# Performance work log

Measured on AMD Instinct MI355X. Metric: run time of the kernel, lower is better.

## Reference

```python
import jax, jax.numpy as jnp
import numpy as np

B, S, E, H, VS, VT = 128, 256, 512, 512, 32000, 32000


def _lstm_layer(x, mask, Wih, Whh, bih, bhh):
    # x: (S,B,E_in), mask: (S,B) bool. PyTorch gate order i,f,g,o.
    h0 = jnp.zeros((x.shape[1], Whh.shape[1]), x.dtype)
    c0 = h0
    def step(carry, inp):
        h, c = carry
        xt, mt = inp
        g = xt @ Wih.T + h @ Whh.T + bih + bhh
        i, f, gg, o = jnp.split(g, 4, axis=-1)
        i = jax.nn.sigmoid(i); f = jax.nn.sigmoid(f)
        gg = jnp.tanh(gg); o = jax.nn.sigmoid(o)
        c_new = f * c + i * gg
        h_new = o * jnp.tanh(c_new)
        m = mt[:, None]
        h2 = jnp.where(m, h_new, h)
        c2 = jnp.where(m, c_new, c)
        return (h2, c2), jnp.where(m, h_new, 0.0)  # pad_packed zero-pads
    (hT, cT), ys = jax.lax.scan(step, (h0, c0), (x, mask))
    return ys, cT


def setup_inputs() -> dict:
    key = jax.random.key(0)
    ks = jax.random.split(key, 32)
    def w(k, shape, fan_in):
        bound = 1.0 / np.sqrt(fan_in)
        return jax.random.uniform(k, shape, jnp.float32, -bound, bound)
    src_tokens = jax.random.randint(ks[0], (B, S), 0, VS)
    src_lens = jnp.sort(jax.random.randint(ks[1], (B,), S // 2, S + 1))[::-1]
    src_lens = src_lens.at[0].set(S)  # pack_padded expects descending, max = S
    trg_tokens = jax.random.randint(ks[2], (B,), 0, VT)
    inp = {
        'src_tokens': src_tokens, 'src_lens': src_lens, 'trg_tokens': trg_tokens,
        'src_emb': jax.random.normal(ks[3], (VS, E), jnp.float32),
        'trg_emb': jax.random.normal(ks[4], (VT, E), jnp.float32),
        'enc_Wih0': w(ks[5], (4 * H, E), H), 'enc_Whh0': w(ks[6], (4 * H, H), H),
        'enc_bih0': w(ks[7], (4 * H,), H), 'enc_bhh0': w(ks[8], (4 * H,), H),
        'enc_Wih1': w(ks[9], (4 * H, H), H), 'enc_Whh1': w(ks[10], (4 * H, H), H),
        'enc_bih1': w(ks[11], (4 * H,), H), 'enc_bhh1': w(ks[12], (4 * H,), H),
        'dec_Wih': w(ks[13], (4 * H, E + H), H), 'dec_Whh': w(ks[14], (4 * H, H), H),
        'dec_bih': w(ks[15], (4 * H,), H), 'dec_bhh': w(ks[16], (4 * H,), H),
        'W_init': w(ks[17], (H, 2 * H), 2 * H), 'b_init': w(ks[18], (H,), 2 * H),
        'W_hid': w(ks[19], (H, 2 * H), 2 * H), 'b_hid': w(ks[20], (H,), 2 * H),
        'W_out': w(ks[21], (VT, H), H), 'b_out': w(ks[22], (VT,), H),
    }
    return inp


def reference(src_tokens, src_lens, trg_tokens, src_emb, trg_emb,
              enc_Wih0, enc_Whh0, enc_bih0, enc_bhh0,
              enc_Wih1, enc_Whh1, enc_bih1, enc_bhh1,
              dec_Wih, dec_Whh, dec_bih, dec_bhh,
              W_init, b_init, W_hid, b_hid, W_out, b_out):
    # ---- encode ----
    x = src_emb[src_tokens]                       # (B,S,E)
    x = jnp.transpose(x, (1, 0, 2))               # (S,B,E)
    mask = jnp.arange(S)[:, None] < src_lens[None, :]  # (S,B)
    y0, c0f = _lstm_layer(x, mask, enc_Wih0, enc_Whh0, enc_bih0, enc_bhh0)
    y1, c1f = _lstm_layer(y0, mask, enc_Wih1, enc_Whh1, enc_bih1, enc_bhh1)
    src_states = jnp.transpose(y1, (1, 0, 2))     # (B,S,H)
    # final cell states (num_layers,B,H) -> (B, num_layers*H)
    final_cells = jnp.concatenate([c0f, c1f], axis=-1)  # (B,2H)
    c_dec = final_cells @ W_init.T + b_init       # (B,H)
    h_dec = jnp.tanh(c_dec)
    # ---- one decoder step ----
    emb_t = trg_emb[trg_tokens]                   # (B,E)
    vec = jnp.concatenate([emb_t, jnp.zeros((B, H), emb_t.dtype)], axis=-1)
    g = vec @ dec_Wih.T + h_dec @ dec_Whh.T + dec_bih + dec_bhh
    i, f, gg, o = jnp.split(g, 4, axis=-1)
    c = jax.nn.sigmoid(f) * c_dec + jax.nn.sigmoid(i) * jnp.tanh(gg)
    h = jax.nn.sigmoid(o) * jnp.tanh(c)           # (B,H)
    # ---- masked dot attention ----
    scores = jnp.einsum('bsh,bh->bs', src_states, h)
    smask = jnp.arange(S)[None, :] < src_lens[:, None]
    scores = jnp.where(smask, scores, -jnp.inf)
    attw = jax.nn.softmax(scores, axis=-1)
    context = jnp.einsum('bs,bsh->bh', attw, src_states)
    attn_vec = jnp.concatenate([h, context], axis=-1) @ W_hid.T + b_hid
    logits = attn_vec @ W_out.T + b_out
    prd_token = jnp.argmax(logits, axis=-1)       # softmax is monotone
    return context, h, prd_token
```

## Files before the change

kernel.cpp:

```cpp
#include <hip/hip_runtime.h>
#include <stdint.h>


typedef _Float16 f16;
typedef f16 f16x8 __attribute__((ext_vector_type(8)));
typedef float f32x4 __attribute__((ext_vector_type(4)));

#define LOSCALE 2048.0f
#define LOINV   (1.0f/2048.0f)

#define B_  128
#define S_  256
#define H_  512

__device__ __forceinline__ uint16_t hbits(f16 h){ union{ f16 f; uint16_t u; } c; c.f=h; return c.u; }

__device__ __forceinline__ uint32_t split_ph2(float x){
  f16 h = (f16)x;
  float r = (x - (float)h) * LOSCALE;
  return (uint32_t)hbits(h) | ((uint32_t)hbits((f16)r) << 16);
}
__device__ __forceinline__ float ph2val(uint32_t p){
  union{ uint16_t u; f16 f; } a, b; a.u = (uint16_t)p; b.u = (uint16_t)(p>>16);
  return (float)a.f + (float)b.f * LOINV;
}

__device__ __forceinline__ void pack_hi_lo(const uint4& a, const uint4& b, uint4& hi, uint4& lo){
  hi = make_uint4((a.x & 0xffffu) | (a.y << 16),
                  (a.z & 0xffffu) | (a.w << 16),
                  (b.x & 0xffffu) | (b.y << 16),
                  (b.z & 0xffffu) | (b.w << 16));
  lo = make_uint4((a.x >> 16) | (a.y & 0xffff0000u),
                  (a.z >> 16) | (a.w & 0xffff0000u),
                  (b.x >> 16) | (b.y & 0xffff0000u),
                  (b.z >> 16) | (b.w & 0xffff0000u));
}

__device__ __forceinline__ void split_pack8(const float* x, uint4& hi, uint4& lo){
  uint16_t h[8], l[8];
#pragma unroll
  for (int e = 0; e < 8; ++e) {
    f16 hh = (f16)x[e];
    float r = (x[e] - (float)hh) * LOSCALE;
    h[e] = hbits(hh); l[e] = hbits((f16)r);
  }
  hi = make_uint4((uint32_t)h[0]|((uint32_t)h[1]<<16), (uint32_t)h[2]|((uint32_t)h[3]<<16),
                  (uint32_t)h[4]|((uint32_t)h[5]<<16), (uint32_t)h[6]|((uint32_t)h[7]<<16));
  lo = make_uint4((uint32_t)l[0]|((uint32_t)l[1]<<16), (uint32_t)l[2]|((uint32_t)l[3]<<16),
                  (uint32_t)l[4]|((uint32_t)l[5]<<16), (uint32_t)l[6]|((uint32_t)l[7]<<16));
}

__device__ __forceinline__ f32x4 mfma16(uint4 a, uint4 b, f32x4 c){
  return __builtin_amdgcn_mfma_f32_16x16x32_f16(
      __builtin_bit_cast(f16x8, a), __builtin_bit_cast(f16x8, b), c, 0, 0, 0);
}

__device__ __forceinline__ float sigm(float x){ return 1.0f/(1.0f + expf(-x)); }
__device__ __forceinline__ float fsigm(float x){ return 1.0f/(1.0f + __expf(-x)); }
__device__ __forceinline__ float ftanh(float x){
  float ax = fabsf(x);
  float e = __expf(-2.0f*ax);
  float r = (1.0f - e)/(1.0f + e);
  return copysignf(r, x);
}

__device__ __forceinline__ uint32_t plane_word(uint32_t p, uint32_t pp, int odd){
  return odd ? ((pp >> 16) | (p & 0xffff0000u))
             : ((p & 0xffffu) | (pp << 16));
}

__device__ __forceinline__ size_t fl_idx(int row, int k){
  return (size_t)(k >> 5) * 4096 + (size_t)(row >> 4) * 512 + (size_t)(k & 1) * 256
       + (size_t)((k >> 3) & 3) * 64 + (size_t)(row & 15) * 4 + (size_t)((k & 7) >> 1);
}

__device__ __forceinline__ void gload_lds16(const uint32_t* gbase, uint32_t* lbase, int lane){
#if __has_builtin(__builtin_amdgcn_global_load_lds)
  __builtin_amdgcn_global_load_lds(
      (const __attribute__((address_space(1))) uint32_t*)(gbase + lane*4),
      (__attribute__((address_space(3))) uint32_t*)lbase, 16, 0, 0);
#else
  *(uint4*)(lbase + lane*4) = *(const uint4*)(gbase + lane*4);
#endif
}

__global__ __launch_bounds__(256) void k_embed_src_fl(const int* __restrict__ tok,
    const float* __restrict__ emb, uint32_t* __restrict__ out)
{
  const size_t total = (size_t)S_ * B_ * H_;
  for (size_t i = (size_t)blockIdx.x*256 + threadIdx.x; i < total; i += (size_t)gridDim.x*256) {
    int s = (int)(i >> 16), b = (int)((i >> 9) & 127), k = (int)(i & 511);
    int t = tok[b*S_ + s];
    uint32_t p = split_ph2(emb[(size_t)t*H_ + k]);
    uint32_t pp = __shfl_xor(p, 1);
    out[(size_t)s*65536 + fl_idx(b, k)] = plane_word(p, pp, k & 1);
  }
}

__global__ __launch_bounds__(256) void k_embed_trg(const int* __restrict__ tok,
    const float* __restrict__ emb, uint32_t* __restrict__ out)
{
  int i = blockIdx.x*256 + threadIdx.x;
  int e = i & (H_-1), b = i >> 9;
  int t = tok[b];
  out[i] = split_ph2(emb[(size_t)t*H_ + e]);
}

__global__ __launch_bounds__(256) void k_packW(const float* __restrict__ W,
    uint32_t* __restrict__ out)
{
  int i = blockIdx.x*256 + threadIdx.x;
  int n = i >> 9, k = i & 511;
  uint32_t p = split_ph2(W[i]);
  uint32_t pp = __shfl_xor(p, 1);
  out[(size_t)(n >> 7)*65536 + fl_idx(n & 127, k)] = plane_word(p, pp, k & 1);
}

__global__ __launch_bounds__(256) void k_packAfl(const float* __restrict__ a,
    uint32_t* __restrict__ out)
{
  int i = blockIdx.x*256 + threadIdx.x;
  int b = i >> 9, k = i & 511;
  uint32_t p = split_ph2(a[i]);
  uint32_t pp = __shfl_xor(p, 1);
  out[fl_idx(b, k)] = plane_word(p, pp, k & 1);
}

__global__ __launch_bounds__(256,2) void k_gemm_fl(
    const uint32_t* __restrict__ Afl,
    const uint32_t* __restrict__ Wfl,
    const float* __restrict__ b0, const float* __restrict__ b1,
    float* __restrict__ C, int N, int addC)
{
  __shared__ uint8_t sm[65536];
  const int tid = threadIdx.x, lane = tid & 63, wv = tid >> 6;
  const int wm = wv >> 1, wn = wv & 1;
  const int bn0 = blockIdx.x * 128, bm0 = blockIdx.y * 128;
  const uint32_t* Ab = Afl + (size_t)blockIdx.y * 65536;
  const uint32_t* Wb = Wfl + (size_t)blockIdx.x * 65536;

  f32x4 acc0[4][4], acc1[4][4];
#pragma unroll
  for (int i = 0; i < 4; ++i)
#pragma unroll
    for (int j = 0; j < 4; ++j) { acc0[i][j] = (f32x4){0,0,0,0}; acc1[i][j] = (f32x4){0,0,0,0}; }

  for (int it = 0; it < 8; ++it) {
    __syncthreads();
    {
      const uint32_t* gsrc = (wv < 2 ? Ab : Wb) + (size_t)it*8192 + (size_t)(wv & 1)*4096;
      uint32_t* lb = (uint32_t*)(sm + (size_t)wv*16384);
#pragma unroll
      for (int e = 0; e < 16; ++e)
        gload_lds16(gsrc + e*256, lb + e*256, lane);
    }
    asm volatile("s_waitcnt vmcnt(0)" ::: "memory");
    __syncthreads();

#pragma unroll
    for (int kt = 0; kt < 2; ++kt) {
      uint4 ah[4], al[4];
#pragma unroll
      for (int i = 0; i < 4; ++i) {
        const uint8_t* p = sm + (size_t)(kt*8 + wm*4 + i)*2048 + lane*16;
        ah[i] = *(const uint4*)p; al[i] = *(const uint4*)(p + 1024);
      }
#pragma unroll
      for (int j = 0; j < 4; ++j) {
        const uint8_t* p = sm + 32768 + (size_t)(kt*8 + wn*4 + j)*2048 + lane*16;
        uint4 bh = *(const uint4*)p;
        uint4 bl = *(const uint4*)(p + 1024);
#pragma unroll
        for (int i = 0; i < 4; ++i) {
          acc0[i][j] = mfma16(ah[i], bh, acc0[i][j]);
          acc1[i][j] = mfma16(al[i], bh, acc1[i][j]);
          acc1[i][j] = mfma16(ah[i], bl, acc1[i][j]);
        }
      }
    }
  }

#pragma unroll
  for (int i = 0; i < 4; ++i) {
    int row0 = bm0 + (wm*4+i)*16 + ((lane>>4)<<2);
#pragma unroll
    for (int j = 0; j < 4; ++j) {
      int col = bn0 + (wn*4+j)*16 + (lane & 15);
      float bias = 0.f;
      if (b0) bias += b0[col];
      if (b1) bias += b1[col];
      f32x4 v = acc0[i][j] + acc1[i][j] * LOINV;
#pragma unroll
      for (int r = 0; r < 4; ++r) {
        size_t idx = (size_t)(row0 + r) * N + col;
        float out = v[r] + bias;
        if (addC) out += C[idx];
        C[idx] = out;
      }
    }
  }
}

__global__ __launch_bounds__(256,2) void k_gemm(
    const uint32_t* __restrict__ A, int lda,
    const float* __restrict__ W, int ldw,
    const float* __restrict__ b0, const float* __restrict__ b1,
    float* __restrict__ C, int N, int K, int addC)
{
  __shared__ uint8_t sm[65536];
  const int tid = threadIdx.x;
  const int lane = tid & 63, wv = tid >> 6;
  const int wm = wv >> 1, wn = wv & 1;
  const int bn0 = blockIdx.x * 128, bm0 = blockIdx.y * 128;

  const int srow = tid >> 1;
  const int skh  = (tid & 1) * 32;
  const int smt  = srow >> 4, sr = srow & 15, skt = tid & 1;

  f32x4 acc0[4][4], acc1[4][4];
#pragma unroll
  for (int i = 0; i < 4; ++i)
#pragma unroll
    for (int j = 0; j < 4; ++j) { acc0[i][j] = (f32x4){0,0,0,0}; acc1[i][j] = (f32x4){0,0,0,0}; }

  for (int k0 = 0; k0 < K; k0 += 64) {
    __syncthreads();
    {
      const uint32_t* ap = A + (size_t)(bm0 + srow) * lda + (k0 + skh);
      uint4 q[8];
#pragma unroll
      for (int e = 0; e < 8; ++e) q[e] = *(const uint4*)(ap + e*4);
#pragma unroll
      for (int kg = 0; kg < 4; ++kg) {
        uint4 hi, lo; pack_hi_lo(q[2*kg], q[2*kg+1], hi, lo);
        uint8_t* dst = sm + (size_t)(smt*2 + skt)*2048 + (size_t)(sr + 16*kg)*16;
        *(uint4*)dst = hi; *(uint4*)(dst + 1024) = lo;
      }
    }
    {
      const float* wp = W + (size_t)(bn0 + srow) * ldw + (k0 + skh);
      float xs[32];
#pragma unroll
      for (int e = 0; e < 8; ++e) { float4 v = *(const float4*)(wp + e*4);
        xs[e*4+0]=v.x; xs[e*4+1]=v.y; xs[e*4+2]=v.z; xs[e*4+3]=v.w; }
#pragma unroll
      for (int kg = 0; kg < 4; ++kg) {
        uint4 hi, lo; split_pack8(xs + kg*8, hi, lo);
        uint8_t* dst = sm + 32768 + (size_t)(smt*2 + skt)*2048 + (size_t)(sr + 16*kg)*16;
        *(uint4*)dst = hi; *(uint4*)(dst + 1024) = lo;
      }
    }
    __syncthreads();

#pragma unroll
    for (int kt = 0; kt < 2; ++kt) {
      uint4 ah[4], al[4];
#pragma unroll
      for (int i = 0; i < 4; ++i) {
        const uint8_t* p = sm + (size_t)(((wm*4+i)*2 + kt))*2048 + lane*16;
        ah[i] = *(const uint4*)p; al[i] = *(const uint4*)(p + 1024);
      }
#pragma unroll
      for (int j = 0; j < 4; ++j) {
        const uint8_t* p = sm + 32768 + (size_t)(((wn*4+j)*2 + kt))*2048 + lane*16;
        uint4 bh = *(const uint4*)p;
        uint4 bl = *(const uint4*)(p + 1024);
#pragma unroll
        for (int i = 0; i < 4; ++i) {
          acc0[i][j] = mfma16(ah[i], bh, acc0[i][j]);
          acc1[i][j] = mfma16(al[i], bh, acc1[i][j]);
          acc1[i][j] = mfma16(ah[i], bl, acc1[i][j]);
        }
      }
    }
  }

#pragma unroll
  for (int i = 0; i < 4; ++i) {
    int row0 = bm0 + (wm*4+i)*16 + ((lane>>4)<<2);
#pragma unroll
    for (int j = 0; j < 4; ++j) {
      int col = bn0 + (wn*4+j)*16 + (lane & 15);
      float bias = 0.f;
      if (b0) bias += b0[col];
      if (b1) bias += b1[col];
      f32x4 v = acc0[i][j] + acc1[i][j] * LOINV;
#pragma unroll
      for (int r = 0; r < 4; ++r) {
        size_t idx = (size_t)(row0 + r) * N + col;
        float out = v[r] + bias;
        if (addC) out += C[idx];
        C[idx] = out;
      }
    }
  }
}

__global__ __launch_bounds__(256,1) void k_lstm2(
    const float* __restrict__ Whh0, const float* __restrict__ Whh1,
    const float* __restrict__ bih1, const float* __restrict__ bhh1,
    const float* __restrict__ xg,
    const int*  __restrict__ lens,
    uint32_t* __restrict__ mb0,
    uint32_t* __restrict__ mb1,
    float* __restrict__ cb0, float* __restrict__ cb1,
    uint32_t* __restrict__ y1buf,
    uint32_t* __restrict__ flg0, uint32_t* __restrict__ flg1,
    const uint32_t* __restrict__ Wp1,
    int s0, int nt)
{
  __shared__ uint8_t sm[163840];
  uint8_t* wih = sm;
  uint8_t* tile = sm + 131072;
  uint64_t* tile64 = (uint64_t*)tile;
  float* g0ex = (float*)tile;
  float* g1ex = (float*)(tile + 4096);

  const int tid = threadIdx.x, lane = tid & 63, wv = tid >> 6;
  const int bg = blockIdx.x & 7, hs = blockIdx.x >> 3;
  const int row = lane & 15, qh = lane >> 4;

  {
    const uint32_t* wpb = Wp1 + (size_t)(wv*4 + (hs >> 3))*65536 + (size_t)(hs & 7)*512;
    uint32_t* lb = (uint32_t*)(wih + (size_t)wv*32768);
#pragma unroll
    for (int kt = 0; kt < 16; ++kt) {
      gload_lds16(wpb + kt*4096,       lb + kt*512,       lane);
      gload_lds16(wpb + kt*4096 + 256, lb + kt*512 + 256, lane);
    }
  }

  uint4 w0h[16], w0l[16], w1h[16], w1l[16];
  {
    const float* r0 = Whh0 + (size_t)(wv*512 + hs*16 + row)*512 + qh*8;
    const float* r1 = Whh1 + (size_t)(wv*512 + hs*16 + row)*512 + qh*8;
#pragma unroll
    for (int kt = 0; kt < 16; ++kt) {
      float xs[8];
      float4 v0 = *(const float4*)(r0 + kt*32), v1 = *(const float4*)(r0 + kt*32 + 4);
      xs[0]=v0.x; xs[1]=v0.y; xs[2]=v0.z; xs[3]=v0.w;
      xs[4]=v1.x; xs[5]=v1.y; xs[6]=v1.z; xs[7]=v1.w;
      split_pack8(xs, w0h[kt], w0l[kt]);
      v0 = *(const float4*)(r1 + kt*32); v1 = *(const float4*)(r1 + kt*32 + 4);
      xs[0]=v0.x; xs[1]=v0.y; xs[2]=v0.z; xs[3]=v0.w;
      xs[4]=v1.x; xs[5]=v1.y; xs[6]=v1.z; xs[7]=v1.w;
      split_pack8(xs, w1h[kt], w1l[kt]);
    }
  }

  const int b_l = tid >> 4, uu = tid & 15;
  const int bglob = bg*16 + b_l;
  const size_t bgoff = (size_t)bg*8192;
  const int oct_p = hs*2 + (uu >> 3);
  const size_t widx = (size_t)b_l*512 + (size_t)(uu & 1)*256
                    + ((size_t)(oct_p ^ b_l) << 2) + (size_t)((uu & 7) >> 1);
  const int len_b = lens[bglob];
  const int lenA  = lens[bg*16 + row];
  float c0_reg = cb0[(size_t)bglob*512 + hs*16 + uu];
  float c1_reg = cb1[(size_t)bglob*512 + hs*16 + uu];
  float h0_reg, h1_reg;
  {
    size_t ib = (size_t)(s0 & 1)*65536 + bgoff + (size_t)b_l*512
              + ((size_t)(oct_p ^ b_l) << 2) + (size_t)((uu & 7) >> 1);
    uint32_t hiw = mb0[ib], low = mb0[ib + 256];
    int sh = (uu & 1) * 16;
    union{ uint16_t u; f16 f; } ch, cl;
    ch.u = (uint16_t)(hiw >> sh); cl.u = (uint16_t)(low >> sh);
    h0_reg = (float)ch.f + (float)cl.f * LOINV;
    int s1i = (s0 >= 1) ? (s0 - 1) : 0;
    size_t ib1 = (size_t)(s1i & 1)*65536 + bgoff + (size_t)b_l*512
               + ((size_t)(oct_p ^ b_l) << 2) + (size_t)((uu & 7) >> 1);
    hiw = mb1[ib1]; low = mb1[ib1 + 256];
    ch.u = (uint16_t)(hiw >> sh); cl.u = (uint16_t)(low >> sh);
    h1_reg = (float)ch.f + (float)cl.f * LOINV;
  }
  float b1g[4];
#pragma unroll
  for (int g = 0; g < 4; ++g)
    b1g[g] = bih1[g*512 + hs*16 + uu] + bhh1[g*512 + hs*16 + uu];
  const size_t yfl = (size_t)(hs >> 1)*4096 + (size_t)bg*512 + (size_t)(uu & 1)*256
                   + (size_t)((((hs & 1) << 1) | (uu >> 3)))*64 + (size_t)b_l*4
                   + (size_t)((uu & 7) >> 1);

  asm volatile("s_waitcnt vmcnt(0)" ::: "memory");
  __syncthreads();

  for (int it = 0; it < nt; ++it) {
    const int t = s0 + it;
    const bool aL0 = (t < 256);
    const bool aL1 = (t > 0);

    float xv0 = 0.f, xv1 = 0.f, xv2 = 0.f, xv3 = 0.f;
    if (aL0) {
      const float* xgp = xg + ((size_t)it*128 + bglob)*2048 + hs*16 + uu;
      xv0 = xgp[0]; xv1 = xgp[512]; xv2 = xgp[1024]; xv3 = xgp[1536];
    }

    if (it > 0 && wv == 0) {
      const uint32_t* fp = flg0 + bg*32 + (lane & 31);
      while (1) {
        uint32_t f = __hip_atomic_load(fp, __ATOMIC_RELAXED, __HIP_MEMORY_SCOPE_SYSTEM);
        if (__all((int)(f >= (uint32_t)t))) break;
        __builtin_amdgcn_s_sleep(1);
      }
    }
    __syncthreads();

    {
      const uint64_t* src = (const uint64_t*)(mb0 + (size_t)(t & 1)*65536 + bgoff);
      uint64_t v[16];
#pragma unroll
      for (int e = 0; e < 16; ++e)
        v[e] = __hip_atomic_load(src + tid + e*256, __ATOMIC_RELAXED, __HIP_MEMORY_SCOPE_SYSTEM);
#pragma unroll
      for (int e = 0; e < 16; ++e)
        tile64[tid + e*256] = v[e];
    }
    __syncthreads();

    f32x4 A0 = (f32x4){0,0,0,0}, A1 = (f32x4){0,0,0,0}, A2 = (f32x4){0,0,0,0};
    f32x4 B0 = (f32x4){0,0,0,0}, B1 = (f32x4){0,0,0,0}, B2 = (f32x4){0,0,0,0};
    {
      const uint8_t* hrp = tile + (size_t)row*2048;
      const uint8_t* wbase = wih + (size_t)wv*32768;
      const bool cY = aL1 && ((t - 1) < lenA);
      const uint4 z4 = make_uint4(0,0,0,0);
#pragma unroll
      for (int kt = 0; kt < 16; ++kt) {
        int oct = kt*4 + qh;
        const uint8_t* pA = hrp + (((oct ^ row)) << 4);
        uint4 ah = *(const uint4*)pA, al = *(const uint4*)(pA + 1024);
        A0 = mfma16(ah, w0h[kt], A0);
        A1 = mfma16(al, w0h[kt], A1);
        A2 = mfma16(ah, w0l[kt], A2);
        uint4 yh = cY ? ah : z4, yl = cY ? al : z4;
        const uint8_t* pB = wbase + (size_t)kt*2048 + lane*16;
        uint4 bh = *(const uint4*)pB, bl = *(const uint4*)(pB + 1024);
        B0 = mfma16(yh, bh, B0);
        B1 = mfma16(yl, bh, B1);
        B2 = mfma16(yh, bl, B2);
      }
    }
    if (aL1 && it > 0 && wv == 0) {
      const uint32_t* fp = flg1 + bg*32 + (lane & 31);
      while (1) {
        uint32_t f = __hip_atomic_load(fp, __ATOMIC_RELAXED, __HIP_MEMORY_SCOPE_SYSTEM);
        if (__all((int)(f >= (uint32_t)(t - 1)))) break;
        __builtin_amdgcn_s_sleep(1);
      }
    }
    __syncthreads();

    if (aL1) {
      const uint64_t* src = (const uint64_t*)(mb1 + (size_t)((t - 1) & 1)*65536 + bgoff);
      uint64_t v[16];
#pragma unroll
      for (int e = 0; e < 16; ++e)
        v[e] = __hip_atomic_load(src + tid + e*256, __ATOMIC_RELAXED, __HIP_MEMORY_SCOPE_SYSTEM);
#pragma unroll
      for (int e = 0; e < 16; ++e)
        tile64[tid + e*256] = v[e];
    }
    __syncthreads();

    if (aL1) {
      const uint8_t* hrp = tile + (size_t)row*2048;
#pragma unroll
      for (int kt = 0; kt < 16; ++kt) {
        int oct = kt*4 + qh;
        const uint8_t* pA = hrp + (((oct ^ row)) << 4);
        uint4 ah = *(const uint4*)pA, al = *(const uint4*)(pA + 1024);
        B0 = mfma16(ah, w1h[kt], B0);
        B1 = mfma16(al, w1h[kt], B1);
        B2 = mfma16(ah, w1l[kt], B2);
      }
    }
    __syncthreads();

    {
      int col = lane & 15, rb = (lane >> 4) << 2;
      if (aL0) {
#pragma unroll
        for (int r = 0; r < 4; ++r)
          g0ex[(size_t)(wv*16 + rb + r)*16 + col] = A0[r] + (A1[r] + A2[r])*LOINV;
      }
      if (aL1) {
#pragma unroll
        for (int r = 0; r < 4; ++r)
          g1ex[(size_t)(wv*16 + rb + r)*16 + col] = B0[r] + (B1[r] + B2[r])*LOINV;
      }
    }
    __syncthreads();

    uint32_t p1w = 0; bool m1 = false;
    if (aL0) {
      float gi = g0ex[(size_t)(0*16 + b_l)*16 + uu] + xv0;
      float gf = g0ex[(size_t)(1*16 + b_l)*16 + uu] + xv1;
      float gg = g0ex[(size_t)(2*16 + b_l)*16 + uu] + xv2;
      float go = g0ex[(size_t)(3*16 + b_l)*16 + uu] + xv3;
      float cn = fsigm(gf)*c0_reg + fsigm(gi)*ftanh(gg);
      float hn = fsigm(go)*ftanh(cn);
      bool m = (t < len_b);
      c0_reg = m ? cn : c0_reg;
      h0_reg = m ? hn : h0_reg;
      uint32_t p = split_ph2(h0_reg);
      uint32_t pp = __shfl_xor(p, 1);
      __hip_atomic_store(mb0 + (size_t)((t + 1) & 1)*65536 + bgoff + widx,
                         plane_word(p, pp, uu & 1), __ATOMIC_RELAXED, __HIP_MEMORY_SCOPE_SYSTEM);
    }
    if (aL1) {
      float gi = g1ex[(size_t)(0*16 + b_l)*16 + uu] + b1g[0];
      float gf = g1ex[(size_t)(1*16 + b_l)*16 + uu] + b1g[1];
      float gg = g1ex[(size_t)(2*16 + b_l)*16 + uu] + b1g[2];
      float go = g1ex[(size_t)(3*16 + b_l)*16 + uu] + b1g[3];
      float cn = fsigm(gf)*c1_reg + fsigm(gi)*ftanh(gg);
      float hn = fsigm(go)*ftanh(cn);
      m1 = ((t - 1) < len_b);
      c1_reg = m1 ? cn : c1_reg;
      h1_reg = m1 ? hn : h1_reg;
      uint32_t p = split_ph2(h1_reg);
      uint32_t pp = __shfl_xor(p, 1);
      p1w = plane_word(p, pp, uu & 1);
      __hip_atomic_store(mb1 + (size_t)(t & 1)*65536 + bgoff + widx,
                         p1w, __ATOMIC_RELAXED, __HIP_MEMORY_SCOPE_SYSTEM);
    }
    asm volatile("s_waitcnt vmcnt(0)" ::: "memory");
    __syncthreads();
    if (tid == 0) {
      if (aL0) __hip_atomic_store(flg0 + bg*32 + hs, (uint32_t)(t + 1),
                                  __ATOMIC_RELAXED, __HIP_MEMORY_SCOPE_SYSTEM);
      if (aL1) __hip_atomic_store(flg1 + bg*32 + hs, (uint32_t)t,
                                  __ATOMIC_RELAXED, __HIP_MEMORY_SCOPE_SYSTEM);
    }
    if (aL1) y1buf[(size_t)(t - 1)*65536 + yfl] = m1 ? p1w : 0u;
  }
  cb0[(size_t)bglob*512 + hs*16 + uu] = c0_reg;
  cb1[(size_t)bglob*512 + hs*16 + uu] = c1_reg;
}

__global__ __launch_bounds__(256) void k_pack2(const float* __restrict__ a,
    const float* __restrict__ b, uint32_t* __restrict__ out)
{
  int i = blockIdx.x*256 + threadIdx.x;
  int bb = i >> 10, k = i & 1023;
  float x = (k < 512) ? a[(size_t)bb*512 + k] : b[(size_t)bb*512 + k - 512];
  out[i] = split_ph2(x);
}

__global__ __launch_bounds__(256) void k_tanh_split(const float* __restrict__ c,
    uint32_t* __restrict__ hp)
{ int i = blockIdx.x*256 + threadIdx.x; hp[i] = split_ph2(tanhf(c[i])); }

__global__ __launch_bounds__(256) void k_dec_cell(const float* __restrict__ g,
    const float* __restrict__ cdec, float* __restrict__ hout, float* __restrict__ dh)
{
  int i = blockIdx.x*256 + threadIdx.x;
  int b = i >> 9, u = i & 511;
  const float* gb = g + (size_t)b*2048;
  float c = sigm(gb[512 + u])*cdec[i] + sigm(gb[u])*tanhf(gb[1024 + u]);
  float h = sigm(gb[1536 + u])*tanhf(c);
  hout[i] = h; dh[i] = h;
}

__global__ __launch_bounds__(256) void k_attn(const uint32_t* __restrict__ y1,
    const float* __restrict__ h, const int* __restrict__ lens,
    float* __restrict__ ctx, float* __restrict__ dctx)
{
  __shared__ float hsh[512];
  __shared__ float sc[256];
  __shared__ float red[8];
  const int b = blockIdx.x, tid = threadIdx.x, lane = tid & 63, wv = tid >> 6;
  hsh[tid]       = h[(size_t)b*512 + tid];
  hsh[tid + 256] = h[(size_t)b*512 + tid + 256];
  const int len = lens[b];
  __syncthreads();

  const size_t lanebase = (size_t)(lane >> 2)*4096 + (size_t)(b >> 4)*512
                        + (size_t)(lane & 3)*64 + (size_t)(b & 15)*4;
  for (int it = 0; it < 64; ++it) {
    int s = wv*64 + it;
    const uint32_t* yb = y1 + (size_t)s*65536 + lanebase;
    uint4 hw = *(const uint4*)yb;
    uint4 lw = *(const uint4*)(yb + 256);
    int k0 = lane*8;
    uint32_t hws[4] = {hw.x,hw.y,hw.z,hw.w}, lws[4] = {lw.x,lw.y,lw.z,lw.w};
    float d = 0.f;
#pragma unroll
    for (int w = 0; w < 4; ++w) {
      union{uint16_t u; f16 f;} h0,h1,l0,l1;
      h0.u=(uint16_t)hws[w]; h1.u=(uint16_t)(hws[w]>>16);
      l0.u=(uint16_t)lws[w]; l1.u=(uint16_t)(lws[w]>>16);
      d += ((float)h0.f + (float)l0.f*LOINV) * hsh[k0 + 2*w]
         + ((float)h1.f + (float)l1.f*LOINV) * hsh[k0 + 2*w + 1];
    }
    for (int off = 32; off; off >>= 1) d += __shfl_xor(d, off);
    if (lane == 0) sc[s] = d;
  }
  __syncthreads();

  float v = (tid < len) ? sc[tid] : -INFINITY;
  float mx = v;
  for (int off = 32; off; off >>= 1) mx = fmaxf(mx, __shfl_xor(mx, off));
  if (lane == 0) red[wv] = mx;
  __syncthreads();
  mx = fmaxf(fmaxf(red[0], red[1]), fmaxf(red[2], red[3]));
  float e = (tid < len) ? expf(v - mx) : 0.f;
  float ssum = e;
  for (int off = 32; off; off >>= 1) ssum += __shfl_xor(ssum, off);
  if (lane == 0) red[4 + wv] = ssum;
  __syncthreads();
  float tot = red[4] + red[5] + red[6] + red[7];
  __syncthreads();
  sc[tid] = e / tot;
  __syncthreads();

  const int u0 = tid, u1 = tid + 256;
  const size_t bu0 = (size_t)(u0 >> 5)*4096 + (size_t)(b >> 4)*512
                   + (size_t)((u0 >> 3) & 3)*64 + (size_t)(b & 15)*4 + (size_t)((u0 & 7) >> 1);
  const size_t bu1 = (size_t)(u1 >> 5)*4096 + (size_t)(b >> 4)*512
                   + (size_t)((u1 >> 3) & 3)*64 + (size_t)(b & 15)*4 + (size_t)((u1 & 7) >> 1);
  const int sh = (tid & 1) * 16;
  float acc0 = 0.f, acc1 = 0.f;
  for (int s = 0; s < 256; ++s) {
    float w = sc[s];
    const uint32_t* yb = y1 + (size_t)s*65536;
    uint32_t hi0 = yb[bu0], lo0 = yb[bu0 + 256];
    uint32_t hi1 = yb[bu1], lo1 = yb[bu1 + 256];
    union{uint16_t u; f16 f;} a,b2,c2,d2;
    a.u =(uint16_t)(hi0 >> sh); b2.u=(uint16_t)(lo0 >> sh);
    c2.u=(uint16_t)(hi1 >> sh); d2.u=(uint16_t)(lo1 >> sh);
    acc0 += w*((float)a.f  + (float)b2.f*LOINV);
    acc1 += w*((float)c2.f + (float)d2.f*LOINV);
  }
  ctx [(size_t)b*512 + tid]       = acc0;  ctx [(size_t)b*512 + tid + 256] = acc1;
  dctx[(size_t)b*512 + tid]       = acc0;  dctx[(size_t)b*512 + tid + 256] = acc1;
}

__global__ __launch_bounds__(256) void k_argmax(const float* __restrict__ logits,
    float* __restrict__ out)
{
  __shared__ float bv[256];
  __shared__ int   bi[256];
  const int b = blockIdx.x, tid = threadIdx.x;
  const float* L = logits + (size_t)b*32000;
  float best = -INFINITY; int idx = 0;
  for (int i = tid; i < 32000; i += 256) {
    float v = L[i];
    if (v > best) { best = v; idx = i; }
  }
  bv[tid] = best; bi[tid] = idx;
  __syncthreads();
  for (int sft = 128; sft; sft >>= 1) {
    if (tid < sft) {
      if (bv[tid+sft] > bv[tid] || (bv[tid+sft] == bv[tid] && bi[tid+sft] < bi[tid])) {
        bv[tid] = bv[tid+sft]; bi[tid] = bi[tid+sft];
      }
    }
    __syncthreads();
  }
  if (tid == 0) out[b] = (float)bi[0];
}

extern "C" void kernel_launch(void* const* d_in, const int* in_sizes, int n_in,
                              void* d_out, int out_size, void* d_ws, size_t ws_size,
                              hipStream_t stream)
{
  (void)in_sizes; (void)n_in; (void)out_size; (void)ws_size;
  const int*   src_tokens = (const int*)  d_in[0];
  const int*   src_lens   = (const int*)  d_in[1];
  const int*   trg_tokens = (const int*)  d_in[2];
  const float* src_emb    = (const float*)d_in[3];
  const float* trg_emb    = (const float*)d_in[4];
  const float* Wih0 = (const float*)d_in[5];
  const float* Whh0 = (const float*)d_in[6];
  const float* bih0 = (const float*)d_in[7];
  const float* bhh0 = (const float*)d_in[8];
  const float* Wih1 = (const float*)d_in[9];
  const float* Whh1 = (const float*)d_in[10];
  const float* bih1 = (const float*)d_in[11];
  const float* bhh1 = (const float*)d_in[12];
  const float* dWih = (const float*)d_in[13];
  const float* dWhh = (const float*)d_in[14];
  const float* dbih = (const float*)d_in[15];
  const float* dbhh = (const float*)d_in[16];
  const float* Winit= (const float*)d_in[17];
  const float* binit= (const float*)d_in[18];
  const float* Whid = (const float*)d_in[19];
  const float* bhid = (const float*)d_in[20];
  const float* Wout = (const float*)d_in[21];
  const float* bout = (const float*)d_in[22];

  uint8_t* ws = (uint8_t*)d_ws;
  constexpr size_t MBs = 1ull << 20;
  constexpr size_t OFF_AP    = 0;
  constexpr size_t OFF_Y1    = 64*MBs;
  constexpr size_t OFF_XG    = 128*MBs;
  constexpr size_t OFF_MB    = 192*MBs;
  constexpr size_t OFF_CB0   = OFF_MB    + 1*MBs;
  constexpr size_t OFF_CB1   = OFF_CB0   + 256*1024;
  constexpr size_t OFF_FLG   = OFF_CB1   + 256*1024;
  constexpr size_t OFF_PK    = OFF_FLG   + 4096;
  constexpr size_t OFF_CDEC  = OFF_PK    + 512*1024;
  constexpr size_t OFF_HDECP = OFF_CDEC  + 256*1024;
  constexpr size_t OFF_EMBP  = OFF_HDECP + 256*1024;
  constexpr size_t OFF_G     = OFF_EMBP  + 256*1024;
  constexpr size_t OFF_HDEC2 = OFF_G     + 1*MBs;
  constexpr size_t OFF_CTX   = OFF_HDEC2 + 256*1024;
  constexpr size_t OFF_AVEC  = OFF_CTX   + 256*1024;
  constexpr size_t OFF_AVECP = OFF_AVEC  + 256*1024;
  constexpr size_t OFF_LOG   = OFF_AVECP + 256*1024;

  uint32_t* Ap    = (uint32_t*)(ws + OFF_AP);
  uint32_t* Y1    = (uint32_t*)(ws + OFF_Y1);
  float*    Xg    = (float*)   (ws + OFF_XG);
  uint32_t* WoutF = (uint32_t*)(ws + OFF_XG);
  uint32_t* mb0   = (uint32_t*)(ws + OFF_MB);
  uint32_t* mb1   = (uint32_t*)(ws + OFF_MB + 512*1024);
  float*    cb0   = (float*)   (ws + OFF_CB0);
  float*    cb1   = (float*)   (ws + OFF_CB1);
  uint32_t* flg0  = (uint32_t*)(ws + OFF_FLG);
  uint32_t* flg1  = (uint32_t*)(ws + OFF_FLG + 2048);
  uint32_t* pk    = (uint32_t*)(ws + OFF_PK);
  float*    cdec  = (float*)   (ws + OFF_CDEC);
  uint32_t* hdecp = (uint32_t*)(ws + OFF_HDECP);
  uint32_t* embp  = (uint32_t*)(ws + OFF_EMBP);
  float*    g     = (float*)   (ws + OFF_G);
  float*    hdec2 = (float*)   (ws + OFF_HDEC2);
  float*    ctx   = (float*)   (ws + OFF_CTX);
  float*    avec  = (float*)   (ws + OFF_AVEC);
  uint32_t* avecp = (uint32_t*)(ws + OFF_AVECP);
  float*    logit = (float*)   (ws + OFF_LOG);
  uint32_t* Wp0   = (uint32_t*)(ws + OFF_LOG);
  uint32_t* Wp1   = (uint32_t*)(ws + OFF_LOG + 4*MBs);
  float*    dout  = (float*)   d_out;

  k_packW<<<4096, 256, 0, stream>>>(Wih0, Wp0);
  k_packW<<<4096, 256, 0, stream>>>(Wih1, Wp1);

  hipMemsetAsync(mb0,  0, 1024*1024, stream);
  hipMemsetAsync(flg0, 0, 4096, stream);
  hipMemsetAsync(cb0,  0, 65536*4, stream);
  hipMemsetAsync(cb1,  0, 65536*4, stream);
  k_embed_src_fl<<<2048, 256, 0, stream>>>(src_tokens, src_emb, Ap);
  for (int c = 0; c < 4; ++c) {
    int s0 = c * 64;
    k_gemm_fl<<<dim3(16, 64), 256, 0, stream>>>(Ap + (size_t)s0*65536,
        Wp0, bih0, bhh0, Xg, 2048, 0);
    k_lstm2<<<256, 256, 0, stream>>>(Whh0, Whh1, bih1, bhh1, Xg, src_lens,
        mb0, mb1, cb0, cb1, Y1, flg0, flg1, Wp1, s0, (c == 3) ? 65 : 64);
  }

  k_packW<<<64000, 256, 0, stream>>>(Wout, WoutF);

  k_pack2<<<512, 256, 0, stream>>>(cb0, cb1, pk);
  k_gemm<<<dim3(4, 1), 256, 0, stream>>>(pk, 1024, Winit, 1024, binit, nullptr,
      cdec, 512, 1024, 0);
  k_tanh_split<<<256, 256, 0, stream>>>(cdec, hdecp);

  k_embed_trg<<<256, 256, 0, stream>>>(trg_tokens, trg_emb, embp);
  k_gemm<<<dim3(16, 1), 256, 0, stream>>>(embp, 512, dWih, 1024, dbih, dbhh,
      g, 2048, 512, 0);
  k_gemm<<<dim3(16, 1), 256, 0, stream>>>(hdecp, 512, dWhh, 512, nullptr, nullptr,
      g, 2048, 512, 1);
  k_dec_cell<<<256, 256, 0, stream>>>(g, cdec, hdec2, dout + 65536);

  k_attn<<<128, 256, 0, stream>>>(Y1, hdec2, src_lens, ctx, dout);

  k_pack2<<<512, 256, 0, stream>>>(hdec2, ctx, pk);
  k_gemm<<<dim3(4, 1), 256, 0, stream>>>(pk, 1024, Whid, 1024, bhid, nullptr,
      avec, 512, 1024, 0);
  k_packAfl<<<256, 256, 0, stream>>>(avec, avecp);
  k_gemm_fl<<<dim3(250, 1), 256, 0, stream>>>(avecp, WoutF, bout, nullptr,
      logit, 32000, 0);
  k_argmax<<<128, 256, 0, stream>>>(logit, dout + 131072);
}
```

Measured before the change: 2.485 ms.

## Poll both layer flags up front and prefetch layer-1 state before layer-0 MFMAs

Both flag spin-waits (layer 0 on wave 0, layer 1 on wave 1) now run concurrently before the first barrier, and the global loads of the layer-1 hidden state are issued together with the layer-0 loads. The layer-1 data is held in registers and written to LDS after the layer-0 matmul, which hides its fetch latency behind the MFMAs. __syncthreads is replaced by raw s_barrier with explicit lgkmcnt waits and sched_barriers, which cuts unnecessary vmcnt waits. The trade is more register pressure (32 extra uint64 values) and a longer wait, because layer 1 must now be ready before layer 0 can proceed.

Result: no change. 2.484 ms (-0.0%).

```diff
diff --git a/kernel.cpp b/kernel.cpp
--- a/kernel.cpp
+++ b/kernel.cpp
@@ -396,27 +396,43 @@
       xv0 = xgp[0]; xv1 = xgp[512]; xv2 = xgp[1024]; xv3 = xgp[1536];
     }
 
-    if (it > 0 && wv == 0) {
-      const uint32_t* fp = flg0 + bg*32 + (lane & 31);
-      while (1) {
-        uint32_t f = __hip_atomic_load(fp, __ATOMIC_RELAXED, __HIP_MEMORY_SCOPE_SYSTEM);
-        if (__all((int)(f >= (uint32_t)t))) break;
-        __builtin_amdgcn_s_sleep(1);
-      }
-    }
-    __syncthreads();
-
-    {
-      const uint64_t* src = (const uint64_t*)(mb0 + (size_t)(t & 1)*65536 + bgoff);
-      uint64_t v[16];
+    if (it > 0) {
+      if (wv == 0) {
+        const uint32_t* fp = flg0 + bg*32 + (lane & 31);
+        while (1) {
+          uint32_t f = __hip_atomic_load(fp, __ATOMIC_RELAXED, __HIP_MEMORY_SCOPE_SYSTEM);
+          if (__all((int)(f >= (uint32_t)t))) break;
+          __builtin_amdgcn_s_sleep(1);
+        }
+      } else if (wv == 1) {
+        const uint32_t* fp = flg1 + bg*32 + (lane & 31);
+        while (1) {
+          uint32_t f = __hip_atomic_load(fp, __ATOMIC_RELAXED, __HIP_MEMORY_SCOPE_SYSTEM);
+          if (__all((int)(f >= (uint32_t)(t - 1)))) break;
+          __builtin_amdgcn_s_sleep(1);
+        }
+      }
+    }
+    __builtin_amdgcn_s_barrier();
+    __builtin_amdgcn_sched_barrier(0);
+
+    const uint64_t* sp0 = (const uint64_t*)(mb0 + (size_t)(t & 1)*65536 + bgoff);
+    const uint64_t* sp1 = (const uint64_t*)(mb1 + (size_t)((t - 1) & 1)*65536 + bgoff);
+    uint64_t v0[16], v1[16];
+#pragma unroll
+    for (int e = 0; e < 16; ++e)
+      v0[e] = __hip_atomic_load(sp0 + tid + e*256, __ATOMIC_RELAXED, __HIP_MEMORY_SCOPE_SYSTEM);
+    if (aL1) {
 #pragma unroll
       for (int e = 0; e < 16; ++e)
-        v[e] = __hip_atomic_load(src + tid + e*256, __ATOMIC_RELAXED, __HIP_MEMORY_SCOPE_SYSTEM);
-#pragma unroll
-      for (int e = 0; e < 16; ++e)
-        tile64[tid + e*256] = v[e];
-    }
-    __syncthreads();
+        v1[e] = __hip_atomic_load(sp1 + tid + e*256, __ATOMIC_RELAXED, __HIP_MEMORY_SCOPE_SYSTEM);
+    }
+#pragma unroll
+    for (int e = 0; e < 16; ++e)
+      tile64[tid + e*256] = v0[e];
+    asm volatile("s_waitcnt lgkmcnt(0)" ::: "memory");
+    __builtin_amdgcn_s_barrier();
+    __builtin_amdgcn_sched_barrier(0);
 
     f32x4 A0 = (f32x4){0,0,0,0}, A1 = (f32x4){0,0,0,0}, A2 = (f32x4){0,0,0,0};
     f32x4 B0 = (f32x4){0,0,0,0}, B1 = (f32x4){0,0,0,0}, B2 = (f32x4){0,0,0,0};
@@ -441,27 +457,18 @@
         B2 = mfma16(yh, bl, B2);
       }
     }
-    if (aL1 && it > 0 && wv == 0) {
-      const uint32_t* fp = flg1 + bg*32 + (lane & 31);
-      while (1) {
-        uint32_t f = __hip_atomic_load(fp, __ATOMIC_RELAXED, __HIP_MEMORY_SCOPE_SYSTEM);
-        if (__all((int)(f >= (uint32_t)(t - 1)))) break;
-        __builtin_amdgcn_s_sleep(1);
-      }
-    }
-    __syncthreads();
+    __builtin_amdgcn_sched_barrier(0);
+    __builtin_amdgcn_s_barrier();
+    __builtin_amdgcn_sched_barrier(0);
 
     if (aL1) {
-      const uint64_t* src = (const uint64_t*)(mb1 + (size_t)((t - 1) & 1)*65536 + bgoff);
-      uint64_t v[16];
 #pragma unroll
       for (int e = 0; e < 16; ++e)
-        v[e] = __hip_atomic_load(src + tid + e*256, __ATOMIC_RELAXED, __HIP_MEMORY_SCOPE_SYSTEM);
-#pragma unroll
-      for (int e = 0; e < 16; ++e)
-        tile64[tid + e*256] = v[e];
-    }
-    __syncthreads();
+        tile64[tid + e*256] = v1[e];
+    }
+    asm volatile("s_waitcnt lgkmcnt(0)" ::: "memory");
+    __builtin_amdgcn_s_barrier();
+    __builtin_amdgcn_sched_barrier(0);
 
     if (aL1) {
       const uint8_t* hrp = tile + (size_t)row*2048;
@@ -475,7 +482,9 @@
         B2 = mfma16(ah, w1l[kt], B2);
       }
     }
-    __syncthreads();
+    __builtin_amdgcn_sched_barrier(0);
+    __builtin_amdgcn_s_barrier();
+    __builtin_amdgcn_sched_barrier(0);
 
     {
       int col = lane & 15, rb = (lane >> 4) << 2;
@@ -490,7 +499,9 @@
           g1ex[(size_t)(wv*16 + rb + r)*16 + col] = B0[r] + (B1[r] + B2[r])*LOINV;
       }
     }
-    __syncthreads();
+    asm volatile("s_waitcnt lgkmcnt(0)" ::: "memory");
+    __builtin_amdgcn_s_barrier();
+    __builtin_amdgcn_sched_barrier(0);
 
     uint32_t p1w = 0; bool m1 = false;
     if (aL0) {
@@ -525,7 +536,8 @@
                          p1w, __ATOMIC_RELAXED, __HIP_MEMORY_SCOPE_SYSTEM);
     }
     asm volatile("s_waitcnt vmcnt(0)" ::: "memory");
-    __syncthreads();
+    __builtin_amdgcn_s_barrier();
+    __builtin_amdgcn_sched_barrier(0);
     if (tid == 0) {
       if (aL0) __hip_atomic_store(flg0 + bg*32 + hs, (uint32_t)(t + 1),
                                   __ATOMIC_RELAXED, __HIP_MEMORY_SCOPE_SYSTEM);
```
